# Optimization experiments

Measured on AMD Instinct MI355X. Metric: run time of the kernel, lower is better.

Reference implementation:

```python
import jax, jax.numpy as jnp
import numpy as np

B, N, F_IN, F_OUT = 8, 2048, 128, 64
ALPHA = 0.2  # LeakyReLU negative slope
NEG_INF = -9e15


def setup_inputs() -> dict:
    key = jax.random.key(0)
    k1, k2, k3, k4 = jax.random.split(key, 4)
    h = jax.random.normal(k1, (B, N, F_IN), dtype=jnp.float32)
    adj = jax.random.randint(k2, (B, N, N), 0, 2, dtype=jnp.int32)
    # xavier_uniform with gain=1.414 approximated by scaled normals (values are arbitrary params)
    W = jax.random.normal(k3, (F_IN, F_OUT), dtype=jnp.float32) * (1.414 * np.sqrt(2.0 / (F_IN + F_OUT)))
    a = jax.random.normal(k4, (2 * F_OUT, 1), dtype=jnp.float32) * (1.414 * np.sqrt(2.0 / (2 * F_OUT + 1)))
    return {"h": h, "adj": adj, "W": W, "a": a}


def reference(h, adj, W, a):
    # Wh: [B, N, F_out]
    Wh = jnp.einsum('bnf,fo->bno', h, W)
    Fo = W.shape[1]
    a1 = a[:Fo, 0]   # [F_out]
    a2 = a[Fo:, 0]   # [F_out]
    # e[b,i,j] = leakyrelu(Wh[b,i]@a1 + Wh[b,j]@a2)  (== cat(Wh_i,Wh_j)@a, same math, no N^2*2F blowup)
    e1 = jnp.einsum('bno,o->bn', Wh, a1)  # [B, N]
    e2 = jnp.einsum('bno,o->bn', Wh, a2)  # [B, N]
    e = e1[:, :, None] + e2[:, None, :]   # [B, N, N]
    e = jnp.where(e > 0, e, ALPHA * e)    # LeakyReLU
    e = jnp.where(adj > 0, e, NEG_INF)    # mask non-edges
    attention = jax.nn.softmax(e, axis=-1)
    # dropout is identity in inference mode (deterministic reference)
    h_prime = jnp.einsum('bij,bjo->bio', attention, Wh)  # [B, N, F_out]
    return jax.nn.elu(h_prime)  # concat=True branch
```

## Files before the change

kernel.cpp:

```cpp
#include <hip/hip_runtime.h>
#include <hip/hip_bf16.h>

#define BB 8
#define NN 2048
#define FIN 128
#define FO 64
#define ALPHA 0.2f

typedef __attribute__((ext_vector_type(8))) short bf16x8;
typedef __attribute__((ext_vector_type(4))) float f32x4;
typedef __attribute__((ext_vector_type(4))) int i32x4;

__device__ inline short f2bf(float x) {
    unsigned u = __float_as_uint(x);
    u += 0x7fffu + ((u >> 16) & 1u);
    return (short)(u >> 16);
}

__global__ __launch_bounds__(256) void wh_kernel(
    const float* __restrict__ h, const float* __restrict__ W,
    const float* __restrict__ a, float* __restrict__ e1, float* __restrict__ e2,
    float* __restrict__ e2p, short* __restrict__ whF)
{
    const int t  = threadIdx.x;
    const int o  = t & 63;
    const int wv = t >> 6;
    const int r0 = blockIdx.x * 32;
    const float* __restrict__ hrow =
        h + (size_t)(r0 + __builtin_amdgcn_readfirstlane(wv) * 8) * FIN;

    float acc[8];
#pragma unroll
    for (int rr = 0; rr < 8; rr++) acc[rr] = 0.f;

    for (int f = 0; f < FIN; f += 4) {
        const float w0 = W[(f + 0) * FO + o];
        const float w1 = W[(f + 1) * FO + o];
        const float w2 = W[(f + 2) * FO + o];
        const float w3 = W[(f + 3) * FO + o];
#pragma unroll
        for (int rr = 0; rr < 8; rr++) {
            const float4 hv = *(const float4*)(hrow + rr * FIN + f);
            acc[rr] = fmaf(hv.x, w0, acc[rr]);
            acc[rr] = fmaf(hv.y, w1, acc[rr]);
            acc[rr] = fmaf(hv.z, w2, acc[rr]);
            acc[rr] = fmaf(hv.w, w3, acc[rr]);
        }
    }

    const int b   = r0 / NN;
    const int ib0 = r0 - b * NN;
    const int ibb = ib0 + wv * 8;
    const int jc  = ibb >> 5;
    const int qq  = (ibb >> 3) & 3;
    const int ot  = o >> 4, mm = o & 15;
    const int L   = mm + qq * 16;
    bf16x8 frag;
#pragma unroll
    for (int rr = 0; rr < 8; rr++) frag[rr] = f2bf(acc[rr]);
    *(bf16x8*)(whF + ((((size_t)(b * 64 + jc) * 4 + ot) * 64 + L) * 8)) = frag;

    const float a1 = a[o], a2 = a[FO + o];
    float vmax = -3.0e38f;
#pragma unroll
    for (int rr = 0; rr < 8; rr++) {
        float v1 = acc[rr] * a1, v2 = acc[rr] * a2;
#pragma unroll
        for (int msk = 32; msk >= 1; msk >>= 1) {
            v1 += __shfl_xor(v1, msk, 64);
            v2 += __shfl_xor(v2, msk, 64);
        }
        vmax = fmaxf(vmax, v2);
        if (o == 0) { e1[r0 + wv * 8 + rr] = v1; e2[r0 + wv * 8 + rr] = v2; }
    }
    if (o == 0) e2p[b * 256 + (ib0 >> 5) * 4 + wv] = vmax;
}

struct SMemC { float comb[4][16][64]; float lsum[4][16]; float red4[4]; };

#define SB(K) (((K) >> 1) * 256 + ((K) & 1) * 32)

__global__ __launch_bounds__(256, 4) void attn_kernel(
    const int* __restrict__ adj, const float* __restrict__ e1,
    const float* __restrict__ e2, const float* __restrict__ e2p,
    const short* __restrict__ whF, float* __restrict__ out)
{
    __shared__ SMemC sm;
    const int t = threadIdx.x, w = t >> 6, lane = t & 63;
    const int m = lane & 15, q = lane >> 4;
    const int blk = blockIdx.x;
    const int b  = blk >> 7;
    const int i0 = (blk & 127) * 16;
    const int i  = i0 + m;

    float pv = e2p[b * 256 + t];
    const float e1v = e1[b * NN + i];
#pragma unroll
    for (int k = 32; k >= 1; k >>= 1) pv = fmaxf(pv, __shfl_xor(pv, k, 64));
    if (lane == 0) sm.red4[w] = pv;
    __syncthreads();
    const float e2mx = fmaxf(fmaxf(sm.red4[0], sm.red4[1]),
                             fmaxf(sm.red4[2], sm.red4[3]));

    float mi = e1v + e2mx;
    mi = mi > 0.f ? mi : ALPHA * mi;

    const short* whFb = whF + (size_t)b * (64 * 4 * 64 * 8);
    const int* arow = adj + ((size_t)(b * NN + i)) * NN + w * 64 + q * 8;
    const float* e2b = e2 + b * NN;

    f32x4 acc0 = {0.f,0.f,0.f,0.f}, acc1 = acc0, acc2 = acc0, acc3 = acc0;
    float lsum = 0.f;

    i32x4 aj0[4], aj1[4];
    bf16x8 wb[2][4];
    f32x4  eb[2][2];

    {
        const short* bfp = whFb + (size_t)((SB(0) + w * 64) >> 5) * 2048 + lane * 8;
        wb[0][0] = *(const bf16x8*)(bfp);
        wb[0][1] = *(const bf16x8*)(bfp + 512);
        wb[0][2] = *(const bf16x8*)(bfp + 1024);
        wb[0][3] = *(const bf16x8*)(bfp + 1536);
        const float* ew = e2b + SB(0) + w * 64 + q * 8;
        eb[0][0] = *(const f32x4*)(ew);
        eb[0][1] = *(const f32x4*)(ew + 4);
    }
    asm volatile("" ::: "memory");
#pragma unroll
    for (int k = 0; k < 4; k++) {
        aj0[k] = *(const i32x4*)(arow + SB(k));
        aj1[k] = *(const i32x4*)(arow + SB(k) + 4);
    }
    asm volatile("" ::: "memory");

#pragma unroll
    for (int k = 0; k < 16; k++) {
        if (k < 15) {
            const int sbn = SB(k + 1);
            const short* bfp = whFb + (size_t)((sbn + w * 64) >> 5) * 2048 + lane * 8;
            wb[(k + 1) & 1][0] = *(const bf16x8*)(bfp);
            wb[(k + 1) & 1][1] = *(const bf16x8*)(bfp + 512);
            wb[(k + 1) & 1][2] = *(const bf16x8*)(bfp + 1024);
            wb[(k + 1) & 1][3] = *(const bf16x8*)(bfp + 1536);
            const float* ew = e2b + sbn + w * 64 + q * 8;
            eb[(k + 1) & 1][0] = *(const f32x4*)(ew);
            eb[(k + 1) & 1][1] = *(const f32x4*)(ew + 4);
        }
        asm volatile("" ::: "memory");

        {
            bf16x8 af;
#pragma unroll
            for (int jj = 0; jj < 8; jj++) {
                const int   av  = (jj < 4) ? aj0[k & 3][jj] : aj1[k & 3][jj - 4];
                const float e2j = (jj < 4) ? eb[k & 1][0][jj] : eb[k & 1][1][jj - 4];
                float e = e1v + e2j;
                e = e > 0.f ? e : ALPHA * e;
                const float pe = (av > 0) ? __expf(e - mi) : 0.f;
                lsum += pe;
                af[jj] = f2bf(pe);
            }
            acc0 = __builtin_amdgcn_mfma_f32_16x16x32_bf16(af, wb[k & 1][0], acc0, 0, 0, 0);
            acc1 = __builtin_amdgcn_mfma_f32_16x16x32_bf16(af, wb[k & 1][1], acc1, 0, 0, 0);
            acc2 = __builtin_amdgcn_mfma_f32_16x16x32_bf16(af, wb[k & 1][2], acc2, 0, 0, 0);
            acc3 = __builtin_amdgcn_mfma_f32_16x16x32_bf16(af, wb[k & 1][3], acc3, 0, 0, 0);
        }

        if (k < 12) {
            aj0[k & 3] = *(const i32x4*)(arow + SB(k + 4));
            aj1[k & 3] = *(const i32x4*)(arow + SB(k + 4) + 4);
        }
        asm volatile("" ::: "memory");
    }

    lsum += __shfl_xor(lsum, 16, 64);
    lsum += __shfl_xor(lsum, 32, 64);
    if (q == 0) sm.lsum[w][m] = lsum;
#pragma unroll
    for (int ot = 0; ot < 4; ot++) {
        f32x4 av = (ot == 0) ? acc0 : (ot == 1) ? acc1 : (ot == 2) ? acc2 : acc3;
#pragma unroll
        for (int reg = 0; reg < 4; reg++)
            sm.comb[w][q * 4 + reg][ot * 16 + m] = av[reg];
    }
    __syncthreads();

    const int row = t >> 4, c0 = (t & 15) * 4;
    f32x4 sum = *(const f32x4*)&sm.comb[0][row][c0];
#pragma unroll
    for (int ww = 1; ww < 4; ww++) {
        f32x4 sv = *(const f32x4*)&sm.comb[ww][row][c0];
        sum.x += sv.x; sum.y += sv.y; sum.z += sv.z; sum.w += sv.w;
    }
    float l = sm.lsum[0][row] + sm.lsum[1][row] + sm.lsum[2][row] + sm.lsum[3][row];
    l = fmaxf(l, 1e-30f);
    const float rl = 1.f / l;
    float vr[4] = { sum.x * rl, sum.y * rl, sum.z * rl, sum.w * rl };
    f32x4 res;
#pragma unroll
    for (int kk = 0; kk < 4; kk++)
        res[kk] = vr[kk] > 0.f ? vr[kk] : (__expf(vr[kk]) - 1.f);
    *(f32x4*)&out[((size_t)(b * NN + i0 + row)) * FO + c0] = res;
}

extern "C" void kernel_launch(void* const* d_in, const int* in_sizes, int n_in,
                              void* d_out, int out_size, void* d_ws, size_t ws_size,
                              hipStream_t stream) {
    const float* h   = (const float*)d_in[0];
    const int*   adj = (const int*)d_in[1];
    const float* W   = (const float*)d_in[2];
    const float* a   = (const float*)d_in[3];
    float* out = (float*)d_out;

    char* ws = (char*)d_ws;
    short* whF = (short*)ws;
    size_t off = (size_t)BB * 64 * 4 * 64 * 8 * sizeof(short);
    float* e1  = (float*)(ws + off);  off += (size_t)BB * NN * 4;
    float* e2  = (float*)(ws + off);  off += (size_t)BB * NN * 4;
    float* e2p = (float*)(ws + off);

    wh_kernel<<<(BB * NN) / 32, 256, 0, stream>>>(h, W, a, e1, e2, e2p, whF);
    attn_kernel<<<BB * (NN / 16), 256, 0, stream>>>(adj, e1, e2, e2p, whF, out);
}
```

Measured before the change: 233.6 us.

## Stage adjacency tiles through LDS with async global_load_lds pipeline

Replaces per-lane direct register loads of the adjacency matrix with coalesced global-to-LDS async loads (global_load_lds, 4 bytes per lane), staged in a 4-deep ring of 128-column tiles with vmcnt waits and barriers per tile. Each wave loads 4 rows of the 16-row block fully coalesced, then lanes read their 8-element fragments from LDS. The aim is fully contiguous wide reads of the dominant adj stream (N^2 ints) and a deeper prefetch. In exchange it adds a block barrier per tile, LDS usage (about 34KB, unioned with the reduction buffer), and hand-tuned vmcnt counts that must match the issued loads exactly.

```diff
diff --git a/kernel.cpp b/kernel.cpp
--- a/kernel.cpp
+++ b/kernel.cpp
@@ -10,6 +10,13 @@
 typedef __attribute__((ext_vector_type(8))) short bf16x8;
 typedef __attribute__((ext_vector_type(4))) float f32x4;
 typedef __attribute__((ext_vector_type(4))) int i32x4;
+
+typedef __attribute__((address_space(1))) const void gvoid;
+typedef __attribute__((address_space(3))) void lvoid;
+
+__device__ inline void gl_lds4(const void* g, void* l) {
+    __builtin_amdgcn_global_load_lds((gvoid*)g, (lvoid*)l, 4, 0, 0);
+}
 
 __device__ inline short f2bf(float x) {
     unsigned u = __float_as_uint(x);
@@ -76,16 +83,63 @@
     if (o == 0) e2p[b * 256 + (ib0 >> 5) * 4 + wv] = vmax;
 }
 
-struct SMemC { float comb[4][16][64]; float lsum[4][16]; float red4[4]; };
-
-#define SB(K) (((K) >> 1) * 256 + ((K) & 1) * 32)
+struct SMemS { int adj[4][16][132]; };
+struct SMemC { float comb[4][16][64]; float lsum[4][16]; };
+union __align__(16) SMemU { SMemS s; SMemC c; };
+
+#define TILE(T, XW) do {                                                       \
+    asm volatile("s_waitcnt vmcnt(" #XW ")" ::: "memory");                     \
+    __builtin_amdgcn_s_barrier();                                              \
+    if ((T) < 15) {                                                            \
+        const short* bfp = whFb + (size_t)(((T) + 1) * 4 + w) * 2048 + lane * 8;\
+        wb[((T) + 1) & 1][0] = *(const bf16x8*)(bfp);                          \
+        wb[((T) + 1) & 1][1] = *(const bf16x8*)(bfp + 512);                    \
+        wb[((T) + 1) & 1][2] = *(const bf16x8*)(bfp + 1024);                   \
+        wb[((T) + 1) & 1][3] = *(const bf16x8*)(bfp + 1536);                   \
+        const float* ew = e2b + ((T) + 1) * 128 + w * 32 + q * 8;              \
+        eb[((T) + 1) & 1][0] = *(const f32x4*)(ew);                            \
+        eb[((T) + 1) & 1][1] = *(const f32x4*)(ew + 4);                        \
+    }                                                                          \
+    asm volatile("" ::: "memory");           \
+    if ((T) <= 12) {                                                           \
+        _Pragma("unroll")                                                      \
+        for (int rr = 0; rr < 4; rr++) {                                       \
+            gl_lds4(astage + (size_t)rr * NN + ((T) + 3) * 128,                \
+                    &sm.s.adj[((T) + 3) & 3][w * 4 + rr][0]);                  \
+            gl_lds4(astage + (size_t)rr * NN + ((T) + 3) * 128 + 64,           \
+                    &sm.s.adj[((T) + 3) & 3][w * 4 + rr][64]);                 \
+        }                                                                      \
+    }                                                                          \
+    asm volatile("" ::: "memory");                                             \
+    {                                                                          \
+        i32x4 a0 = *(const i32x4*)&sm.s.adj[(T) & 3][m][w * 32 + q * 8];       \
+        i32x4 a1 = *(const i32x4*)&sm.s.adj[(T) & 3][m][w * 32 + q * 8 + 4];   \
+        bf16x8 af;                                                             \
+        _Pragma("unroll")                                                      \
+        for (int jj = 0; jj < 8; jj++) {                                       \
+            const int   av  = (jj < 4) ? a0[jj] : a1[jj - 4];                  \
+            const float e2j = (jj < 4) ? eb[(T) & 1][0][jj]                    \
+                                       : eb[(T) & 1][1][jj - 4];               \
+            float e = e1v + e2j;                                               \
+            e = e > 0.f ? e : ALPHA * e;                                       \
+            const float pe = (av > 0) ? __expf(e - mi) : 0.f;                  \
+            lsum += pe;                                                        \
+            af[jj] = f2bf(pe);                                                 \
+        }                                                                      \
+        acc0 = __builtin_amdgcn_mfma_f32_16x16x32_bf16(af, wb[(T) & 1][0], acc0, 0, 0, 0); \
+        acc1 = __builtin_amdgcn_mfma_f32_16x16x32_bf16(af, wb[(T) & 1][1], acc1, 0, 0, 0); \
+        acc2 = __builtin_amdgcn_mfma_f32_16x16x32_bf16(af, wb[(T) & 1][2], acc2, 0, 0, 0); \
+        acc3 = __builtin_amdgcn_mfma_f32_16x16x32_bf16(af, wb[(T) & 1][3], acc3, 0, 0, 0); \
+    }                                                                          \
+} while (0)
 
 __global__ __launch_bounds__(256, 4) void attn_kernel(
     const int* __restrict__ adj, const float* __restrict__ e1,
     const float* __restrict__ e2, const float* __restrict__ e2p,
     const short* __restrict__ whF, float* __restrict__ out)
 {
-    __shared__ SMemC sm;
+    __shared__ SMemU sm;
+    __shared__ float red4[4];
     const int t = threadIdx.x, w = t >> 6, lane = t & 63;
     const int m = lane & 15, q = lane >> 4;
     const int blk = blockIdx.x;
@@ -97,103 +151,71 @@
     const float e1v = e1[b * NN + i];
 #pragma unroll
     for (int k = 32; k >= 1; k >>= 1) pv = fmaxf(pv, __shfl_xor(pv, k, 64));
-    if (lane == 0) sm.red4[w] = pv;
+    if (lane == 0) red4[w] = pv;
     __syncthreads();
-    const float e2mx = fmaxf(fmaxf(sm.red4[0], sm.red4[1]),
-                             fmaxf(sm.red4[2], sm.red4[3]));
+    const float e2mx = fmaxf(fmaxf(red4[0], red4[1]), fmaxf(red4[2], red4[3]));
 
     float mi = e1v + e2mx;
     mi = mi > 0.f ? mi : ALPHA * mi;
 
     const short* whFb = whF + (size_t)b * (64 * 4 * 64 * 8);
-    const int* arow = adj + ((size_t)(b * NN + i)) * NN + w * 64 + q * 8;
     const float* e2b = e2 + b * NN;
+    const int* astage = adj + (size_t)(b * NN + i0 + w * 4) * NN + lane;
 
     f32x4 acc0 = {0.f,0.f,0.f,0.f}, acc1 = acc0, acc2 = acc0, acc3 = acc0;
     float lsum = 0.f;
 
-    i32x4 aj0[4], aj1[4];
     bf16x8 wb[2][4];
     f32x4  eb[2][2];
 
     {
-        const short* bfp = whFb + (size_t)((SB(0) + w * 64) >> 5) * 2048 + lane * 8;
+        const short* bfp = whFb + (size_t)w * 2048 + lane * 8;
         wb[0][0] = *(const bf16x8*)(bfp);
         wb[0][1] = *(const bf16x8*)(bfp + 512);
         wb[0][2] = *(const bf16x8*)(bfp + 1024);
         wb[0][3] = *(const bf16x8*)(bfp + 1536);
-        const float* ew = e2b + SB(0) + w * 64 + q * 8;
+        const float* ew = e2b + w * 32 + q * 8;
         eb[0][0] = *(const f32x4*)(ew);
         eb[0][1] = *(const f32x4*)(ew + 4);
     }
     asm volatile("" ::: "memory");
 #pragma unroll
-    for (int k = 0; k < 4; k++) {
-        aj0[k] = *(const i32x4*)(arow + SB(k));
-        aj1[k] = *(const i32x4*)(arow + SB(k) + 4);
+    for (int tt = 0; tt < 3; tt++) {
+#pragma unroll
+        for (int rr = 0; rr < 4; rr++) {
+            gl_lds4(astage + (size_t)rr * NN + tt * 128, &sm.s.adj[tt][w * 4 + rr][0]);
+            gl_lds4(astage + (size_t)rr * NN + tt * 128 + 64, &sm.s.adj[tt][w * 4 + rr][64]);
+        }
     }
     asm volatile("" ::: "memory");
 
-#pragma unroll
-    for (int k = 0; k < 16; k++) {
-        if (k < 15) {
-            const int sbn = SB(k + 1);
-            const short* bfp = whFb + (size_t)((sbn + w * 64) >> 5) * 2048 + lane * 8;
-            wb[(k + 1) & 1][0] = *(const bf16x8*)(bfp);
-            wb[(k + 1) & 1][1] = *(const bf16x8*)(bfp + 512);
-            wb[(k + 1) & 1][2] = *(const bf16x8*)(bfp + 1024);
-            wb[(k + 1) & 1][3] = *(const bf16x8*)(bfp + 1536);
-            const float* ew = e2b + sbn + w * 64 + q * 8;
-            eb[(k + 1) & 1][0] = *(const f32x4*)(ew);
-            eb[(k + 1) & 1][1] = *(const f32x4*)(ew + 4);
-        }
-        asm volatile("" ::: "memory");
-
-        {
-            bf16x8 af;
-#pragma unroll
-            for (int jj = 0; jj < 8; jj++) {
-                const int   av  = (jj < 4) ? aj0[k & 3][jj] : aj1[k & 3][jj - 4];
-                const float e2j = (jj < 4) ? eb[k & 1][0][jj] : eb[k & 1][1][jj - 4];
-                float e = e1v + e2j;
-                e = e > 0.f ? e : ALPHA * e;
-                const float pe = (av > 0) ? __expf(e - mi) : 0.f;
-                lsum += pe;
-                af[jj] = f2bf(pe);
-            }
-            acc0 = __builtin_amdgcn_mfma_f32_16x16x32_bf16(af, wb[k & 1][0], acc0, 0, 0, 0);
-            acc1 = __builtin_amdgcn_mfma_f32_16x16x32_bf16(af, wb[k & 1][1], acc1, 0, 0, 0);
-            acc2 = __builtin_amdgcn_mfma_f32_16x16x32_bf16(af, wb[k & 1][2], acc2, 0, 0, 0);
-            acc3 = __builtin_amdgcn_mfma_f32_16x16x32_bf16(af, wb[k & 1][3], acc3, 0, 0, 0);
-        }
-
-        if (k < 12) {
-            aj0[k & 3] = *(const i32x4*)(arow + SB(k + 4));
-            aj1[k & 3] = *(const i32x4*)(arow + SB(k + 4) + 4);
-        }
-        asm volatile("" ::: "memory");
-    }
+    TILE(0, 16);  TILE(1, 22);  TILE(2, 28);  TILE(3, 28);
+    TILE(4, 28);  TILE(5, 28);  TILE(6, 28);  TILE(7, 28);
+    TILE(8, 28);  TILE(9, 28);  TILE(10, 28); TILE(11, 28);
+    TILE(12, 28); TILE(13, 28); TILE(14, 20); TILE(15, 12);
+
+    __syncthreads();
 
     lsum += __shfl_xor(lsum, 16, 64);
     lsum += __shfl_xor(lsum, 32, 64);
-    if (q == 0) sm.lsum[w][m] = lsum;
+    if (q == 0) sm.c.lsum[w][m] = lsum;
 #pragma unroll
     for (int ot = 0; ot < 4; ot++) {
         f32x4 av = (ot == 0) ? acc0 : (ot == 1) ? acc1 : (ot == 2) ? acc2 : acc3;
 #pragma unroll
         for (int reg = 0; reg < 4; reg++)
-            sm.comb[w][q * 4 + reg][ot * 16 + m] = av[reg];
+            sm.c.comb[w][q * 4 + reg][ot * 16 + m] = av[reg];
     }
     __syncthreads();
 
     const int row = t >> 4, c0 = (t & 15) * 4;
-    f32x4 sum = *(const f32x4*)&sm.comb[0][row][c0];
+    f32x4 sum = *(const f32x4*)&sm.c.comb[0][row][c0];
 #pragma unroll
     for (int ww = 1; ww < 4; ww++) {
-        f32x4 sv = *(const f32x4*)&sm.comb[ww][row][c0];
+        f32x4 sv = *(const f32x4*)&sm.c.comb[ww][row][c0];
         sum.x += sv.x; sum.y += sv.y; sum.z += sv.z; sum.w += sv.w;
     }
-    float l = sm.lsum[0][row] + sm.lsum[1][row] + sm.lsum[2][row] + sm.lsum[3][row];
+    float l = sm.c.lsum[0][row] + sm.c.lsum[1][row] + sm.c.lsum[2][row] + sm.c.lsum[3][row];
     l = fmaxf(l, 1e-30f);
     const float rl = 1.f / l;
     float vr[4] = { sum.x * rl, sum.y * rl, sum.z * rl, sum.w * rl };
```

Result: no change. 235.6 us (+0.9%).
